# Optimization experiments

Hardware: AMD Instinct MI355X
Metric: run time of the kernel (lower is better)

The kernel has to match this reference:

```python
import jax, jax.numpy as jnp
import numpy as np

C = 64      # in_channels
H = 32      # hidden_size per direction
K = 8       # kernel_size
L = 4       # num_layers
EPS = 1e-5


def _sru_dir(x, W, v, b, reverse):
    # x: (T, N, in); one SRU direction.
    if reverse:
        x = x[::-1]
    U = x @ W                                   # (T, N, 4H): [candidate z, f_pre, r_pre, highway x']
    z, fp, rp, xp = jnp.split(U, 4, axis=-1)
    vf, vr = jnp.split(v, 2)
    bf, br = jnp.split(b, 2)

    def step(c, inp):
        z_t, fp_t, rp_t, xp_t = inp
        f = jax.nn.sigmoid(fp_t + vf * c + bf)
        r = jax.nn.sigmoid(rp_t + vr * c + br)
        c_new = f * c + (1.0 - f) * z_t
        h = r * c_new + (1.0 - r) * xp_t
        return c_new, h

    c0 = jnp.zeros((x.shape[1], H), x.dtype)
    _, h = jax.lax.scan(step, c0, (z, fp, rp, xp))
    if reverse:
        h = h[::-1]
    return h


def _sru(x, W0, Wr, v, b):
    # Bidirectional multi-layer SRU. x: (T, N, C*K) -> (T, N, 2H)
    Ws = [W0] + [Wr[i] for i in range(Wr.shape[0])]
    h = x
    for l in range(L):
        hf = _sru_dir(h, Ws[l][0], v[l, 0], b[l, 0], False)
        hb = _sru_dir(h, Ws[l][1], v[l, 1], b[l, 1], True)
        h = jnp.concatenate([hf, hb], axis=-1)
    return h


def setup_inputs() -> dict:
    key = jax.random.key(0)
    ks = jax.random.split(key, 8)
    B, Fdim, Tdim = 2, 128, 250
    s = 0.05
    x = jax.random.normal(ks[0], (B, C, Fdim, Tdim), jnp.float32)
    gamma = jnp.ones((C,), jnp.float32)
    beta = jnp.zeros((C,), jnp.float32)
    W0 = jax.random.normal(ks[1], (2, C * K, 4 * H), jnp.float32) * s       # layer 0, 2 dirs
    Wr = jax.random.normal(ks[2], (L - 1, 2, 2 * H, 4 * H), jnp.float32) * s  # layers 1..3
    v = jax.random.normal(ks[3], (L, 2, 2 * H), jnp.float32) * s            # recurrent gate vectors
    b = jnp.zeros((L, 2, 2 * H), jnp.float32)                               # gate biases
    wct = jax.random.normal(ks[4], (2 * H, C, K), jnp.float32) * s          # ConvTranspose1d (in,out,k)
    bct = jnp.zeros((C,), jnp.float32)
    return {"x": x, "gamma": gamma, "beta": beta, "W0": W0, "Wr": Wr,
            "v": v, "b": b, "wct": wct, "bct": bct}


def reference(x, gamma, beta, W0, Wr, v, b, wct, bct):
    x = jnp.swapaxes(x, -1, -2)                 # [B, C, T, F]
    res = x
    B, Cc, T, F = x.shape
    # GroupNorm(num_groups=1): normalize over (C,T,F) per sample, per-channel affine.
    mean = jnp.mean(x, axis=(1, 2, 3), keepdims=True)
    var = jnp.var(x, axis=(1, 2, 3), keepdims=True)
    xn = (x - mean) * jax.lax.rsqrt(var + EPS)
    xn = xn * gamma[None, :, None, None] + beta[None, :, None, None]
    # -> (B*F, C, T), then unfold over T with window K (channel-major block layout).
    xu = jnp.transpose(xn, (0, 3, 1, 2)).reshape(B * F, Cc, T)
    Tn = T - K + 1
    win = jnp.stack([xu[:, :, k:k + Tn] for k in range(K)], axis=2)   # (N, C, K, Tn)
    win = win.reshape(B * F, Cc * K, Tn)
    s = jnp.transpose(win, (2, 0, 1))           # (Tn, N, C*K)
    h = _sru(s, W0, Wr, v, b)                   # (Tn, N, 2H)
    y = jnp.transpose(h, (1, 2, 0))             # (N, 2H, Tn)
    # ConvTranspose1d stride 1 == full correlation with flipped kernel.
    w_conv = jnp.transpose(wct, (1, 0, 2))[:, :, ::-1]                # (out, in, k)
    y = jax.lax.conv_general_dilated(y, w_conv, (1,), [(K - 1, K - 1)],
                                     dimension_numbers=("NCH", "OIH", "NCH"))
    y = y + bct[None, :, None]                  # (N, C, T)
    y = y.reshape(B, F, Cc, T)
    y = jnp.transpose(y, (0, 2, 3, 1))          # [B, C, T, F]
    y = y + res
    return jnp.swapaxes(y, -1, -2)              # back to [B, C, F, T]
```

## Files before the change

### kernel.cpp

```cpp
#include <hip/hip_runtime.h>
#include <math.h>

#define Tt 250
#define TnN 243
#define Nn 256
#define EPS_ 1e-5f
#define LOG2E 1.44269504f

typedef unsigned short u16;
typedef __bf16 bf16x8 __attribute__((ext_vector_type(8)));
typedef float f32x4 __attribute__((ext_vector_type(4)));

__device__ __forceinline__ u16 f2bf(float f) {
    unsigned u = __builtin_bit_cast(unsigned, f);
    u += 0x7FFFu + ((u >> 16) & 1u);
    return (u16)(u >> 16);
}
__device__ __forceinline__ float bf2f(u16 s) {
    unsigned u = ((unsigned)s) << 16;
    return __builtin_bit_cast(float, u);
}
__device__ __forceinline__ float hw_exp2(float x) {
    return __builtin_amdgcn_exp2f(x);
}

__device__ __forceinline__ void async_load16(const void* g, void* l) {
    __builtin_amdgcn_global_load_lds(
        (const __attribute__((address_space(1))) unsigned int*)g,
        (__attribute__((address_space(3))) unsigned int*)l, 16, 0, 0);
}

__device__ __forceinline__ void dma72g(const u16* gsrc, int rstride, u16* ldst, int nseg,
                                       int w, int lane, int nw) {
    for (int seg = w; seg < nseg; seg += nw) {
        int c9 = seg * 64 + lane;
        int row = c9 / 9, sub = c9 - row * 9;
        const u16* src = (sub < 8) ? &gsrc[row * rstride + sub * 8] : gsrc;
        async_load16(src, ldst + seg * 512);
    }
}

template<int D>
__device__ __forceinline__ void chain_run(u16* Zr, u16* Fr, float kf, float bf_) {
    bf16x8 z8 = *(const bf16x8*)&Zr[D ? 240 : 0];
    bf16x8 f8 = *(const bf16x8*)&Fr[D ? 240 : 0];
    float c = 0.f;
    for (int grp = 0; grp < 31; ++grp) {
        int gb = D ? (30 - grp) * 8 : grp * 8;
        bf16x8 zn = z8, fn = f8;
        if (grp < 30) {
            int gbn = D ? (29 - grp) * 8 : (grp + 1) * 8;
            zn = *(const bf16x8*)&Zr[gbn];
            fn = *(const bf16x8*)&Fr[gbn];
        }
        bf16x8 co;
        #pragma unroll
        for (int k = 0; k < 8; ++k) {
            const int idx = D ? (7 - k) : k;
            int t = gb + idx;
            float uz = (float)z8[idx];
            float af = -LOG2E * ((float)f8[idx] + bf_);
            float xe = fmaf(kf, c, af);
            float fg = __builtin_amdgcn_rcpf(1.f + hw_exp2(xe));
            float cn = fmaf(fg, c - uz, uz);
            bool ok = (t < TnN);
            if (ok) c = cn;
            co[idx] = ok ? (__bf16)c : (__bf16)0.f;
        }
        *(bf16x8*)&Zr[gb] = co;
        z8 = zn; f8 = fn;
    }
}

__global__ __launch_bounds__(256) void k_prep(const float* __restrict__ x,
                                              const float* __restrict__ W0,
                                              const float* __restrict__ Wr,
                                              const float* __restrict__ wct,
                                              float* __restrict__ stats,
                                              u16* __restrict__ W0k,
                                              u16* __restrict__ Wrt,
                                              u16* __restrict__ Wcto) {
    __shared__ float ls[4], ls2[4];
    const int bx = blockIdx.x, tid = threadIdx.x;
    if (bx < 832) {
        int idx = bx * 256 + tid;
        if (idx < 131072) {
            int k = idx >> 14, j = (idx >> 6) & 255, c = idx & 63;
            int d = j >> 7, ck = c * 8 + k;
            W0k[idx] = f2bf(W0[((size_t)d * 512 + ck) * 128 + (j & 127)]);
        } else if (idx < 180224) {
            int r = idx - 131072;
            int i = r & 63, j = (r >> 6) & 255, lidx = r >> 14;
            Wrt[r] = f2bf(Wr[(size_t)(lidx * 2 + (j >> 7)) * 8192 + i * 128 + (j & 127)]);
        } else {
            int r = idx - 180224;
            int o = r >> 9; int k = r & 511; int kk = k >> 6, ci = k & 63;
            Wcto[r] = f2bf(wct[(size_t)ci * 512 + o * 8 + kk]);
        }
    } else {
        const int sb = bx - 832;
        const int b = sb >> 7;
        const float4* xb = (const float4*)(x + (size_t)b * 64 * 128 * Tt);
        const int n4 = 64 * 128 * Tt / 4;
        float s = 0.f, s2 = 0.f;
        for (int i = (sb & 127) * 256 + tid; i < n4; i += 128 * 256) {
            float4 vv = xb[i];
            s  += vv.x + vv.y + vv.z + vv.w;
            s2 += vv.x * vv.x + vv.y * vv.y + vv.z * vv.z + vv.w * vv.w;
        }
        for (int off = 32; off; off >>= 1) {
            s  += __shfl_down(s, off);
            s2 += __shfl_down(s2, off);
        }
        int lane = tid & 63, w = tid >> 6;
        if (lane == 0) { ls[w] = s; ls2[w] = s2; }
        __syncthreads();
        if (tid == 0) {
            float a = 0.f, a2 = 0.f;
            for (int i = 0; i < 4; i++) { a += ls[i]; a2 += ls2[i]; }
            stats[sb * 2]     = a;
            stats[sb * 2 + 1] = a2;
        }
    }
}

__global__ __launch_bounds__(512) void k_norm(const float* __restrict__ x, const float* __restrict__ stats,
                       const float* __restrict__ gamma, const float* __restrict__ beta,
                       u16* __restrict__ xbt) {
    __shared__ u16 lt[64 * 260];
    __shared__ float sm2[2];
    const int n = blockIdx.x, tid = threadIdx.x;
    const int b = n >> 7, f = n & 127;
    if (tid < 64) {
        float a = 0.f, a2 = 0.f;
        #pragma unroll
        for (int p = 0; p < 2; ++p) {
            int sb = b * 128 + tid + p * 64;
            a  += stats[sb * 2];
            a2 += stats[sb * 2 + 1];
        }
        for (int off = 32; off; off >>= 1) {
            a  += __shfl_down(a, off);
            a2 += __shfl_down(a2, off);
        }
        if (tid == 0) { sm2[0] = a; sm2[1] = a2; }
    }
    __syncthreads();
    const float inv = 1.0f / (float)(64 * 128 * Tt);
    float mean = sm2[0] * inv;
    float var  = sm2[1] * inv - mean * mean;
    float rstd = rsqrtf(var + EPS_);
    const int c = tid >> 3, vq = tid & 7;
    const float gm = gamma[c] * rstd;
    const float bt = beta[c] - mean * gm;
    const float* xr = x + ((size_t)(b * 64 + c) * 128 + f) * Tt;
    #pragma unroll
    for (int j = 0; j < 16; ++j) {
        int t0 = vq * 2 + j * 16;
        unsigned pv = 0u;
        if (t0 < Tt) {
            float2 xv = *(const float2*)&xr[t0];
            pv = (unsigned)f2bf(fmaf(xv.x, gm, bt)) | ((unsigned)f2bf(fmaf(xv.y, gm, bt)) << 16);
        }
        *(unsigned*)&lt[c * 260 + t0] = pv;
    }
    __syncthreads();
    const int cg = tid & 7, tq = tid >> 3;
    #pragma unroll
    for (int it = 0; it < 4; ++it) {
        int t = it * 64 + tq;
        u16 tmp[8];
        #pragma unroll
        for (int jj = 0; jj < 8; ++jj) tmp[jj] = lt[(cg * 8 + jj) * 260 + t];
        uint4 o;
        o.x = (unsigned)tmp[0] | ((unsigned)tmp[1] << 16);
        o.y = (unsigned)tmp[2] | ((unsigned)tmp[3] << 16);
        o.z = (unsigned)tmp[4] | ((unsigned)tmp[5] << 16);
        o.w = (unsigned)tmp[6] | ((unsigned)tmp[7] << 16);
        *(uint4*)&xbt[(size_t)n * 16384 + t * 64 + cg * 8] = o;
    }
}

#define HS0 0
#define ZT0 19008
#define FT0 34880
#define BM0 50752
#define SH_U16 81856
__global__ __launch_bounds__(1024) void k_tail(const u16* __restrict__ XbT,
                                               const u16* __restrict__ W0k,
                                               const u16* __restrict__ Wrt,
                                               const u16* __restrict__ Wc,
                                               const float* __restrict__ v,
                                               const float* __restrict__ bbias,
                                               const float* __restrict__ bct,
                                               const float* __restrict__ x,
                                               float* __restrict__ out) {
    __shared__ __align__(16) u16 sh[SH_U16];
    u16* Hs = sh + HS0;
    u16* ZT = sh + ZT0;
    u16* FT = sh + FT0;
    u16* Bm = sh + BM0;
    const int tid = threadIdx.x;
    const int n = blockIdx.x;
    const int lane = tid & 63, w = tid >> 6;
    const int ml = lane & 15, q = lane >> 4;
    const int b = n >> 7, f = n & 127;
    const int t0 = w * 16 + q * 4;

    for (int lay = 0; lay < 4; ++lay) {
        f32x4 acc[16];
        #pragma unroll
        for (int nt = 0; nt < 16; ++nt) acc[nt] = (f32x4){0.f, 0.f, 0.f, 0.f};

        if (lay == 0) {
            const u16* Xn = XbT + (size_t)n * 16384;
            u16* Bb0 = sh + ZT0;
            u16* Bb1 = Bm;
            dma72g(Xn, 64, Hs, 36, w, lane, 16);
            dma72g(W0k, 64, Bb0, 36, w, lane, 16);
            __syncthreads();
            #pragma unroll
            for (int k = 0; k < 8; ++k) {
                u16* Bl = (k & 1) ? Bb1 : Bb0;
                if (k < 7)
                    dma72g(W0k + (size_t)(k + 1) * 16384, 64, (k & 1) ? Bb0 : Bb1, 36, w, lane, 16);
                #pragma unroll
                for (int c2 = 0; c2 < 2; ++c2) {
                    int c0 = c2 * 32;
                    bf16x8 af = *(const bf16x8*)&Hs[(w * 16 + ml + k) * 72 + c0 + q * 8];
                    #pragma unroll
                    for (int nt = 0; nt < 16; ++nt) {
                        bf16x8 bfr = *(const bf16x8*)&Bl[(nt * 16 + ml) * 72 + c0 + q * 8];
                        acc[nt] = __builtin_amdgcn_mfma_f32_16x16x32_bf16(af, bfr, acc[nt], 0, 0, 0);
                    }
                }
                __syncthreads();
            }
        } else {
            #pragma unroll
            for (int c2 = 0; c2 < 2; ++c2) {
                int c0 = c2 * 32;
                bf16x8 af = *(const bf16x8*)&Hs[(w * 16 + ml + 7) * 72 + c0 + q * 8];
                #pragma unroll
                for (int nt = 0; nt < 16; ++nt) {
                    bf16x8 bfr = *(const bf16x8*)&Bm[(nt * 16 + ml) * 72 + c0 + q * 8];
                    acc[nt] = __builtin_amdgcn_mfma_f32_16x16x32_bf16(af, bfr, acc[nt], 0, 0, 0);
                }
            }
        }

        if (t0 < TnN) {
            bool vec = (t0 + 4 <= TnN);
            #pragma unroll
            for (int d2 = 0; d2 < 2; ++d2)
                #pragma unroll
                for (int j = 0; j < 4; ++j) {
                    int nt = d2 * 8 + j;
                    int g2 = j >> 1, hi = j & 1, hh = hi * 16 + ml;
                    u16* P = (g2 ? FT : ZT) + (d2 * 32 + hh) * 248;
                    if (vec) {
                        uint2 pv;
                        pv.x = (unsigned)f2bf(acc[nt][0]) | ((unsigned)f2bf(acc[nt][1]) << 16);
                        pv.y = (unsigned)f2bf(acc[nt][2]) | ((unsigned)f2bf(acc[nt][3]) << 16);
                        *(uint2*)&P[t0] = pv;
                    } else {
                        #pragma unroll
                        for (int r = 0; r < 4; ++r) {
                            int t = t0 + r;
                            if (t < TnN) P[t] = f2bf(acc[nt][r]);
                        }
                    }
                }
        }
        __syncthreads();

        if (lay < 3) {
            dma72g(Wrt + (size_t)lay * 16384, 64, Bm, 36, w, lane, 16);
        } else {
            #pragma unroll
            for (int i = 0; i < 4; ++i)
                dma72g(Wc + i * 64, 512, Bm + i * 4608, 9, w, lane, 16);
        }

        const float* vv = v + (size_t)(lay * 2) * 64;
        const float* bv = bbias + (size_t)(lay * 2) * 64;

        if (w < 2 && lane < 32) {
            const int d = w, h = lane;
            const float vf = vv[d * 64 + h], bf_ = bv[d * 64 + h];
            const float kf = -LOG2E * vf;
            u16* Zr = &ZT[(d * 32 + h) * 248];
            u16* Fr = &FT[(d * 32 + h) * 248];
            if (d == 0) chain_run<0>(Zr, Fr, kf, bf_);
            else        chain_run<1>(Zr, Fr, kf, bf_);
        }
        __syncthreads();

        if (lay == 0) {
            for (int i = tid; i < 21 * 72; i += 1024) {
                int r = i / 72, ci = i - r * 72;
                int row = r < 7 ? r : (TnN + r);
                Hs[row * 72 + ci] = 0;
            }
        }
        #pragma unroll
        for (int d2 = 0; d2 < 2; ++d2)
            #pragma unroll
            for (int hi = 0; hi < 2; ++hi) {
                int hh = hi * 16 + ml;
                float vr_ = vv[d2 * 64 + 32 + hh], br_ = bv[d2 * 64 + 32 + hh];
                float kr = -LOG2E * vr_;
                const u16* Cr = &ZT[(d2 * 32 + hh) * 248];
                f32x4 rp = acc[d2 * 8 + 4 + hi];
                f32x4 xp = acc[d2 * 8 + 6 + hi];
                #pragma unroll
                for (int r = 0; r < 4; ++r) {
                    int t = t0 + r;
                    if (t < TnN) {
                        float ct = bf2f(Cr[t]);
                        float cpr;
                        if (d2 == 0) cpr = (t == 0) ? 0.f : bf2f(Cr[t - 1]);
                        else         cpr = (t == TnN - 1) ? 0.f : bf2f(Cr[t + 1]);
                        float xr = fmaf(kr, cpr, -LOG2E * (rp[r] + br_));
                        float rg = __builtin_amdgcn_rcpf(1.f + hw_exp2(xr));
                        float hv = fmaf(rg, ct - xp[r], xp[r]);
                        Hs[(t + 7) * 72 + d2 * 32 + hh] = f2bf(hv);
                    }
                }
            }
        __syncthreads();
    }

    {
        u16* T47 = sh + ZT0;
        float* Cf = (float*)(sh + 37440);
        f32x4 cacc[4] = {};
        #pragma unroll
        for (int i = 0; i < 4; ++i)
            dma72g(Wc + (4 + i) * 64, 512, T47 + i * 4608, 9, w, lane, 16);
        #pragma unroll
        for (int m = 0; m < 8; ++m) {
            if (m == 4) __syncthreads();
            const u16* Bl = (m < 4) ? (Bm + m * 4608) : (T47 + (m - 4) * 4608);
            #pragma unroll
            for (int c2 = 0; c2 < 2; ++c2) {
                int ci0 = c2 * 32;
                bf16x8 af = *(const bf16x8*)&Hs[(w * 16 + ml - m + 7) * 72 + ci0 + q * 8];
                #pragma unroll
                for (int nt = 0; nt < 4; ++nt) {
                    bf16x8 bfv = *(const bf16x8*)&Bl[(nt * 16 + ml) * 72 + ci0 + q * 8];
                    cacc[nt] = __builtin_amdgcn_mfma_f32_16x16x32_bf16(af, bfv, cacc[nt], 0, 0, 0);
                }
            }
        }
        __syncthreads();
        float bc[4];
        #pragma unroll
        for (int nt = 0; nt < 4; ++nt) bc[nt] = bct[nt * 16 + ml];
        #pragma unroll
        for (int r = 0; r < 4; ++r) {
            int t = t0 + r;
            if (t < Tt) {
                #pragma unroll
                for (int nt = 0; nt < 4; ++nt)
                    Cf[t * 68 + nt * 16 + ml] = cacc[nt][r] + bc[nt];
            }
        }
        __syncthreads();
        {
            const int sub = tid & 15;
            const int o = tid >> 4;
            const float* xrow = x + ((size_t)(b * 64 + o) * 128 + f) * Tt;
            float* orow = out + ((size_t)(b * 64 + o) * 128 + f) * Tt;
            #pragma unroll
            for (int it = 0; it < 8; ++it) {
                int j = it * 32 + sub * 2;
                if (j < Tt) {
                    float2 xv = *(const float2*)&xrow[j];
                    float2 ov;
                    ov.x = Cf[j * 68 + o] + xv.x;
                    ov.y = Cf[(j + 1) * 68 + o] + xv.y;
                    *(float2*)&orow[j] = ov;
                }
            }
        }
    }
}

extern "C" void kernel_launch(void* const* d_in, const int* in_sizes, int n_in,
                              void* d_out, int out_size, void* d_ws, size_t ws_size,
                              hipStream_t stream) {
    (void)in_sizes; (void)n_in; (void)out_size; (void)ws_size;
    const float* x     = (const float*)d_in[0];
    const float* gamma = (const float*)d_in[1];
    const float* beta  = (const float*)d_in[2];
    const float* W0    = (const float*)d_in[3];
    const float* Wr    = (const float*)d_in[4];
    const float* v     = (const float*)d_in[5];
    const float* bb    = (const float*)d_in[6];
    const float* wct   = (const float*)d_in[7];
    const float* bct   = (const float*)d_in[8];
    float* out = (float*)d_out;

    char* base = (char*)d_ws;
    float* stats = (float*)base;
    u16* W0k  = (u16*)(base + 4096);
    u16* Wrt  = (u16*)(base + 4096 + 262144);
    u16* Wcto = (u16*)(base + 4096 + 262144 + 98304);
    u16* XbT  = (u16*)(base + 4096 + 262144 + 98304 + 65536);

    k_prep<<<dim3(1088), 256, 0, stream>>>(x, W0, Wr, wct, stats, W0k, Wrt, Wcto);
    k_norm<<<dim3(256), 512, 0, stream>>>(x, stats, gamma, beta, XbT);
    k_tail<<<dim3(256), 1024, 0, stream>>>(XbT, W0k, Wrt, Wcto, v, bb, bct, x, out);
}
```

Baseline: 181.7 us.

## Retile SRU projection GEMM to 2x8 warp tiles and move weight conversion into norm kernel

The projection GEMM in k_tail changes from one 16-row M tile by 16 N tiles per warp to two M tiles by eight N tiles, with warps split by direction (wn). Each B fragment loaded from LDS now feeds two MFMAs, so LDS traffic for B roughly halves, while A loads double. Separately, the weight bf16 conversion moves out of the stats kernel and into k_norm, which leaves a smaller stats-only launch. The post-GEMM gate indexing is remapped to match the new per-warp tiling.

```diff
diff --git a/kernel.cpp b/kernel.cpp
--- a/kernel.cpp
+++ b/kernel.cpp
@@ -72,18 +72,61 @@
     }
 }
 
-__global__ __launch_bounds__(256) void k_prep(const float* __restrict__ x,
-                                              const float* __restrict__ W0,
-                                              const float* __restrict__ Wr,
-                                              const float* __restrict__ wct,
-                                              float* __restrict__ stats,
-                                              u16* __restrict__ W0k,
-                                              u16* __restrict__ Wrt,
-                                              u16* __restrict__ Wcto) {
+__global__ __launch_bounds__(256) void k_stats(const float* __restrict__ x,
+                                               float* __restrict__ stats) {
     __shared__ float ls[4], ls2[4];
-    const int bx = blockIdx.x, tid = threadIdx.x;
-    if (bx < 832) {
-        int idx = bx * 256 + tid;
+    const int sb = blockIdx.x, tid = threadIdx.x;
+    const int b = sb >> 7;
+    const float4* xb = (const float4*)(x + (size_t)b * 64 * 128 * Tt);
+    const int n4 = 64 * 128 * Tt / 4;
+    float s = 0.f, s2 = 0.f;
+    for (int i = (sb & 127) * 256 + tid; i < n4; i += 128 * 256) {
+        float4 vv = xb[i];
+        s  += vv.x + vv.y + vv.z + vv.w;
+        s2 += vv.x * vv.x + vv.y * vv.y + vv.z * vv.z + vv.w * vv.w;
+    }
+    for (int off = 32; off; off >>= 1) {
+        s  += __shfl_down(s, off);
+        s2 += __shfl_down(s2, off);
+    }
+    int lane = tid & 63, w = tid >> 6;
+    if (lane == 0) { ls[w] = s; ls2[w] = s2; }
+    __syncthreads();
+    if (tid == 0) {
+        float a = 0.f, a2 = 0.f;
+        for (int i = 0; i < 4; i++) { a += ls[i]; a2 += ls2[i]; }
+        stats[sb * 2]     = a;
+        stats[sb * 2 + 1] = a2;
+    }
+}
+
+__global__ __launch_bounds__(512) void k_norm(const float* __restrict__ x, const float* __restrict__ stats,
+                       const float* __restrict__ gamma, const float* __restrict__ beta,
+                       const float* __restrict__ W0, const float* __restrict__ Wr,
+                       const float* __restrict__ wct,
+                       u16* __restrict__ xbt, u16* __restrict__ W0k,
+                       u16* __restrict__ Wrt, u16* __restrict__ Wcto) {
+    __shared__ u16 lt[64 * 260];
+    __shared__ float sm2[2];
+    const int n = blockIdx.x, tid = threadIdx.x;
+    const int b = n >> 7, f = n & 127;
+    if (tid < 64) {
+        float a = 0.f, a2 = 0.f;
+        #pragma unroll
+        for (int p = 0; p < 2; ++p) {
+            int sb = b * 128 + tid + p * 64;
+            a  += stats[sb * 2];
+            a2 += stats[sb * 2 + 1];
+        }
+        for (int off = 32; off; off >>= 1) {
+            a  += __shfl_down(a, off);
+            a2 += __shfl_down(a2, off);
+        }
+        if (tid == 0) { sm2[0] = a; sm2[1] = a2; }
+    }
+    #pragma unroll
+    for (int it = 0; it < 2; ++it) {
+        int idx = it * 131072 + n * 512 + tid;
         if (idx < 131072) {
             int k = idx >> 14, j = (idx >> 6) & 255, c = idx & 63;
             int d = j >> 7, ck = c * 8 + k;
@@ -92,58 +135,11 @@
             int r = idx - 131072;
             int i = r & 63, j = (r >> 6) & 255, lidx = r >> 14;
             Wrt[r] = f2bf(Wr[(size_t)(lidx * 2 + (j >> 7)) * 8192 + i * 128 + (j & 127)]);
-        } else {
+        } else if (idx < 212992) {
             int r = idx - 180224;
             int o = r >> 9; int k = r & 511; int kk = k >> 6, ci = k & 63;
             Wcto[r] = f2bf(wct[(size_t)ci * 512 + o * 8 + kk]);
         }
-    } else {
-        const int sb = bx - 832;
-        const int b = sb >> 7;
-        const float4* xb = (const float4*)(x + (size_t)b * 64 * 128 * Tt);
-        const int n4 = 64 * 128 * Tt / 4;
-        float s = 0.f, s2 = 0.f;
-        for (int i = (sb & 127) * 256 + tid; i < n4; i += 128 * 256) {
-            float4 vv = xb[i];
-            s  += vv.x + vv.y + vv.z + vv.w;
-            s2 += vv.x * vv.x + vv.y * vv.y + vv.z * vv.z + vv.w * vv.w;
-        }
-        for (int off = 32; off; off >>= 1) {
-            s  += __shfl_down(s, off);
-            s2 += __shfl_down(s2, off);
-        }
-        int lane = tid & 63, w = tid >> 6;
-        if (lane == 0) { ls[w] = s; ls2[w] = s2; }
-        __syncthreads();
-        if (tid == 0) {
-            float a = 0.f, a2 = 0.f;
-            for (int i = 0; i < 4; i++) { a += ls[i]; a2 += ls2[i]; }
-            stats[sb * 2]     = a;
-            stats[sb * 2 + 1] = a2;
-        }
-    }
-}
-
-__global__ __launch_bounds__(512) void k_norm(const float* __restrict__ x, const float* __restrict__ stats,
-                       const float* __restrict__ gamma, const float* __restrict__ beta,
-                       u16* __restrict__ xbt) {
-    __shared__ u16 lt[64 * 260];
-    __shared__ float sm2[2];
-    const int n = blockIdx.x, tid = threadIdx.x;
-    const int b = n >> 7, f = n & 127;
-    if (tid < 64) {
-        float a = 0.f, a2 = 0.f;
-        #pragma unroll
-        for (int p = 0; p < 2; ++p) {
-            int sb = b * 128 + tid + p * 64;
-            a  += stats[sb * 2];
-            a2 += stats[sb * 2 + 1];
-        }
-        for (int off = 32; off; off >>= 1) {
-            a  += __shfl_down(a, off);
-            a2 += __shfl_down(a2, off);
-        }
-        if (tid == 0) { sm2[0] = a; sm2[1] = a2; }
     }
     __syncthreads();
     const float inv = 1.0f / (float)(64 * 128 * Tt);
@@ -204,13 +200,15 @@
     const int n = blockIdx.x;
     const int lane = tid & 63, w = tid >> 6;
     const int ml = lane & 15, q = lane >> 4;
+    const int wm = w >> 1, wn = w & 1;
     const int b = n >> 7, f = n & 127;
-    const int t0 = w * 16 + q * 4;
 
     for (int lay = 0; lay < 4; ++lay) {
-        f32x4 acc[16];
-        #pragma unroll
-        for (int nt = 0; nt < 16; ++nt) acc[nt] = (f32x4){0.f, 0.f, 0.f, 0.f};
+        f32x4 acc[2][8];
+        #pragma unroll
+        for (int mt = 0; mt < 2; ++mt)
+            #pragma unroll
+            for (int nt = 0; nt < 8; ++nt) acc[mt][nt] = (f32x4){0.f, 0.f, 0.f, 0.f};
 
         if (lay == 0) {
             const u16* Xn = XbT + (size_t)n * 16384;
@@ -227,11 +225,16 @@
                 #pragma unroll
                 for (int c2 = 0; c2 < 2; ++c2) {
                     int c0 = c2 * 32;
-                    bf16x8 af = *(const bf16x8*)&Hs[(w * 16 + ml + k) * 72 + c0 + q * 8];
+                    bf16x8 af[2];
                     #pragma unroll
-                    for (int nt = 0; nt < 16; ++nt) {
-                        bf16x8 bfr = *(const bf16x8*)&Bl[(nt * 16 + ml) * 72 + c0 + q * 8];
-                        acc[nt] = __builtin_amdgcn_mfma_f32_16x16x32_bf16(af, bfr, acc[nt], 0, 0, 0);
+                    for (int mt = 0; mt < 2; ++mt)
+                        af[mt] = *(const bf16x8*)&Hs[(wm * 32 + mt * 16 + ml + k) * 72 + c0 + q * 8];
+                    #pragma unroll
+                    for (int nt = 0; nt < 8; ++nt) {
+                        bf16x8 bfr = *(const bf16x8*)&Bl[(wn * 128 + nt * 16 + ml) * 72 + c0 + q * 8];
+                        #pragma unroll
+                        for (int mt = 0; mt < 2; ++mt)
+                            acc[mt][nt] = __builtin_amdgcn_mfma_f32_16x16x32_bf16(af[mt], bfr, acc[mt][nt], 0, 0, 0);
                     }
                 }
                 __syncthreads();
@@ -240,37 +243,43 @@
             #pragma unroll
             for (int c2 = 0; c2 < 2; ++c2) {
                 int c0 = c2 * 32;
-                bf16x8 af = *(const bf16x8*)&Hs[(w * 16 + ml + 7) * 72 + c0 + q * 8];
-                #pragma unroll
-                for (int nt = 0; nt < 16; ++nt) {
-                    bf16x8 bfr = *(const bf16x8*)&Bm[(nt * 16 + ml) * 72 + c0 + q * 8];
-                    acc[nt] = __builtin_amdgcn_mfma_f32_16x16x32_bf16(af, bfr, acc[nt], 0, 0, 0);
-                }
-            }
-        }
-
-        if (t0 < TnN) {
-            bool vec = (t0 + 4 <= TnN);
-            #pragma unroll
-            for (int d2 = 0; d2 < 2; ++d2)
-                #pragma unroll
-                for (int j = 0; j < 4; ++j) {
-                    int nt = d2 * 8 + j;
-                    int g2 = j >> 1, hi = j & 1, hh = hi * 16 + ml;
-                    u16* P = (g2 ? FT : ZT) + (d2 * 32 + hh) * 248;
+                bf16x8 af[2];
+                #pragma unroll
+                for (int mt = 0; mt < 2; ++mt)
+                    af[mt] = *(const bf16x8*)&Hs[(wm * 32 + mt * 16 + ml + 7) * 72 + c0 + q * 8];
+                #pragma unroll
+                for (int nt = 0; nt < 8; ++nt) {
+                    bf16x8 bfr = *(const bf16x8*)&Bm[(wn * 128 + nt * 16 + ml) * 72 + c0 + q * 8];
+                    #pragma unroll
+                    for (int mt = 0; mt < 2; ++mt)
+                        acc[mt][nt] = __builtin_amdgcn_mfma_f32_16x16x32_bf16(af[mt], bfr, acc[mt][nt], 0, 0, 0);
+                }
+            }
+        }
+
+        #pragma unroll
+        for (int mt = 0; mt < 2; ++mt) {
+            int t0 = wm * 32 + mt * 16 + q * 4;
+            if (t0 < TnN) {
+                bool vec = (t0 + 4 <= TnN);
+                #pragma unroll
+                for (int nt = 0; nt < 4; ++nt) {
+                    int g2 = nt >> 1, hh = (nt & 1) * 16 + ml;
+                    u16* P = (g2 ? FT : ZT) + (wn * 32 + hh) * 248;
                     if (vec) {
                         uint2 pv;
-                        pv.x = (unsigned)f2bf(acc[nt][0]) | ((unsigned)f2bf(acc[nt][1]) << 16);
-                        pv.y = (unsigned)f2bf(acc[nt][2]) | ((unsigned)f2bf(acc[nt][3]) << 16);
+                        pv.x = (unsigned)f2bf(acc[mt][nt][0]) | ((unsigned)f2bf(acc[mt][nt][1]) << 16);
+                        pv.y = (unsigned)f2bf(acc[mt][nt][2]) | ((unsigned)f2bf(acc[mt][nt][3]) << 16);
                         *(uint2*)&P[t0] = pv;
                     } else {
                         #pragma unroll
                         for (int r = 0; r < 4; ++r) {
                             int t = t0 + r;
-                            if (t < TnN) P[t] = f2bf(acc[nt][r]);
+                            if (t < TnN) P[t] = f2bf(acc[mt][nt][r]);
                         }
                     }
                 }
+            }
         }
         __syncthreads();
 
@@ -304,36 +313,39 @@
             }
         }
         #pragma unroll
-        for (int d2 = 0; d2 < 2; ++d2)
+        for (int mt = 0; mt < 2; ++mt) {
+            int t0 = wm * 32 + mt * 16 + q * 4;
             #pragma unroll
             for (int hi = 0; hi < 2; ++hi) {
                 int hh = hi * 16 + ml;
-                float vr_ = vv[d2 * 64 + 32 + hh], br_ = bv[d2 * 64 + 32 + hh];
+                float vr_ = vv[wn * 64 + 32 + hh], br_ = bv[wn * 64 + 32 + hh];
                 float kr = -LOG2E * vr_;
-                const u16* Cr = &ZT[(d2 * 32 + hh) * 248];
-                f32x4 rp = acc[d2 * 8 + 4 + hi];
-                f32x4 xp = acc[d2 * 8 + 6 + hi];
+                const u16* Cr = &ZT[(wn * 32 + hh) * 248];
+                f32x4 rp = acc[mt][4 + hi];
+                f32x4 xp = acc[mt][6 + hi];
                 #pragma unroll
                 for (int r = 0; r < 4; ++r) {
                     int t = t0 + r;
                     if (t < TnN) {
                         float ct = bf2f(Cr[t]);
                         float cpr;
-                        if (d2 == 0) cpr = (t == 0) ? 0.f : bf2f(Cr[t - 1]);
+                        if (wn == 0) cpr = (t == 0) ? 0.f : bf2f(Cr[t - 1]);
                         else         cpr = (t == TnN - 1) ? 0.f : bf2f(Cr[t + 1]);
                         float xr = fmaf(kr, cpr, -LOG2E * (rp[r] + br_));
                         float rg = __builtin_amdgcn_rcpf(1.f + hw_exp2(xr));
                         float hv = fmaf(rg, ct - xp[r], xp[r]);
-                        Hs[(t + 7) * 72 + d2 * 32 + hh] = f2bf(hv);
+                        Hs[(t + 7) * 72 + wn * 32 + hh] = f2bf(hv);
                     }
                 }
             }
+        }
         __syncthreads();
     }
 
     {
         u16* T47 = sh + ZT0;
         float* Cf = (float*)(sh + 37440);
+        const int tc0 = w * 16 + q * 4;
         f32x4 cacc[4] = {};
         #pragma unroll
         for (int i = 0; i < 4; ++i)
@@ -359,7 +371,7 @@
         for (int nt = 0; nt < 4; ++nt) bc[nt] = bct[nt * 16 + ml];
         #pragma unroll
         for (int r = 0; r < 4; ++r) {
-            int t = t0 + r;
+            int t = tc0 + r;
             if (t < Tt) {
                 #pragma unroll
                 for (int nt = 0; nt < 4; ++nt)
@@ -409,7 +421,8 @@
     u16* Wcto = (u16*)(base + 4096 + 262144 + 98304);
     u16* XbT  = (u16*)(base + 4096 + 262144 + 98304 + 65536);
 
-    k_prep<<<dim3(1088), 256, 0, stream>>>(x, W0, Wr, wct, stats, W0k, Wrt, Wcto);
-    k_norm<<<dim3(256), 512, 0, stream>>>(x, stats, gamma, beta, XbT);
+    k_stats<<<dim3(256), 256, 0, stream>>>(x, stats);
+    k_norm<<<dim3(256), 512, 0, stream>>>(x, stats, gamma, beta, W0, Wr, wct,
+                                          XbT, W0k, Wrt, Wcto);
     k_tail<<<dim3(256), 1024, 0, stream>>>(XbT, W0k, Wrt, Wcto, v, bb, bct, x, out);
 }
```

Measured after the change: 168.5 us, median of 2. 7.2% less time.
